# Kernel optimization log

Hardware: AMD Instinct MI355X
Metric: run time of the kernel (lower is better)

Reference implementation:

```python
import jax, jax.numpy as jnp
import numpy as np


def setup_inputs() -> dict:
    key = jax.random.key(0)
    k1, k2, k3 = jax.random.split(key, 3)
    B, F0, D = 8192, 39, 16
    L = 128
    hash_x = jax.random.normal(k1, (B, F0, D), dtype=jnp.float32)
    W0 = jax.random.normal(k2, (F0 * F0, L), dtype=jnp.float32) * 0.05
    W1 = jax.random.normal(k3, (F0 * (L // 2), L), dtype=jnp.float32) * 0.05
    return {"hash_x": hash_x, "W0": W0, "W1": W1}


def reference(hash_x, W0, W1):
    # CIN (Compressed Interaction Network) with layer sizes [128, 128], no bias.
    x0 = hash_x                      # [B, F0, D]
    B, F0, D = x0.shape
    L = W0.shape[1]                  # 128

    # --- layer 0 ---
    # outer product over fields per embedding dim: [B, D, F0, F0] -> flatten (i,j) row-major
    z0 = jnp.einsum('bid,bjd->bdij', x0, x0).reshape(B, D, F0 * F0)
    # conv1d with kernel width 1 == matmul over flattened field-pair dim
    cur0 = jax.nn.relu(jnp.einsum('bdk,kl->bld', z0, W0))   # [B, L, D]
    next_h, direct0 = jnp.split(cur0, 2, axis=1)            # each [B, L/2, D]

    # --- layer 1 (final) ---
    Fk = next_h.shape[1]                                     # L/2 = 64
    z1 = jnp.einsum('bid,bjd->bdij', x0, next_h).reshape(B, D, F0 * Fk)
    cur1 = jax.nn.relu(jnp.einsum('bdk,kl->bld', z1, W1))   # [B, L, D]

    result = jnp.concatenate([direct0, cur1], axis=1)        # [B, L/2 + L, D]
    return jnp.sum(result, axis=-1)                          # [B, 192]
```

## Files before the change

### kernel.cpp

```cpp
#include <hip/hip_runtime.h>
#include <hip/hip_bf16.h>


using short8 = __attribute__((ext_vector_type(8))) short;
using f32x4  = __attribute__((ext_vector_type(4))) float;

#define ZSTR 168
#define V_OFF 0
#define Z_OFF 20480
#define H_OFF (20480 + 43008)
#define SMEM_BYTES (20480 + 43008 + 16384)

#define W0_SLICES 50
#define W1_SLICES 80
#define W0PK_ELEMS (W0_SLICES * 8 * 64 * 8)

__device__ __forceinline__ unsigned short f2bf(float x) {
  __hip_bfloat16 h = __float2bfloat16(x);
  return __builtin_bit_cast(unsigned short, h);
}
__device__ __forceinline__ float bf2f(unsigned short b) {
  unsigned int u = ((unsigned int)b) << 16;
  return __builtin_bit_cast(float, u);
}

__global__ void pack_w(const float* __restrict__ W0, const float* __restrict__ W1,
                       unsigned short* __restrict__ wpk) {
  int tid = blockIdx.x * 256 + threadIdx.x;
  if (tid < W0PK_ELEMS) {
    int p = tid >> 7, n = tid & 127;
    int q = p / 160, rem = p - q * 160;
    int ib = rem / 40, j = rem - ib * 40;
    int i = q * 4 + ib;
    float val = (i < 39 && j < 39) ? W0[(i * 39 + j) * 128 + n] : 0.f;
    int s = p >> 5, kl = p & 31;
    int lane = ((kl >> 3) << 4) | (n & 15);
    int ii = kl & 7, nb = n >> 4;
    wpk[((s * 8 + nb) * 64 + lane) * 8 + ii] = f2bf(val);
  } else {
    int t = tid - W0PK_ELEMS;
    if (t < 2560 * 128) {
      int p = t >> 7, n = t & 127;
      int i = p >> 6, j = p & 63;
      float val = (i < 39) ? W1[(i * 64 + j) * 128 + n] : 0.f;
      int s = p >> 5, kl = p & 31;
      int lane = ((kl >> 3) << 4) | (n & 15);
      int ii = kl & 7, nb = n >> 4;
      wpk[W0PK_ELEMS + ((s * 8 + nb) * 64 + lane) * 8 + ii] = f2bf(val);
    }
  }
}

__global__ __launch_bounds__(256) void cin_main(const float* __restrict__ X,
                                                const short8* __restrict__ wpk,
                                                float* __restrict__ out) {
  extern __shared__ char smem[];
  float* V          = (float*)(smem + V_OFF);
  unsigned short* Z = (unsigned short*)(smem + Z_OFF);
  unsigned short* H = (unsigned short*)(smem + H_OFF);

  const int t    = threadIdx.x;
  const int lane = t & 63;
  const int w    = t >> 6;
  const int wm   = w >> 1, wn = w & 1;
  const int l15  = lane & 15, l4 = lane >> 4;
  const int b0   = blockIdx.x * 8;

  const float* xb = X + (size_t)b0 * 624;
  for (int f = t * 4; f < 4992; f += 1024) {
    float4 v4 = *(const float4*)(xb + f);
    int bl = f / 624;
    int rem = f - bl * 624;
    int i = rem >> 4, d0 = rem & 15;
    int r = bl * 16 + d0;
    V[(r + 0) * 40 + i] = v4.x;
    V[(r + 1) * 40 + i] = v4.y;
    V[(r + 2) * 40 + i] = v4.z;
    V[(r + 3) * 40 + i] = v4.w;
  }
  __syncthreads();

  const int rg = t >> 1, hf = t & 1;

  float vj[20];
  #pragma unroll
  for (int jj = 0; jj < 20; jj++) {
    int j = hf * 20 + jj;
    vj[jj] = (j < 39) ? V[rg * 40 + j] : 0.f;
  }

  f32x4 acc[4][4];
  #pragma unroll
  for (int mi = 0; mi < 4; mi++)
    #pragma unroll
    for (int ni = 0; ni < 4; ni++)
      acc[mi][ni] = (f32x4){0.f, 0.f, 0.f, 0.f};

  for (int q = 0; q < 10; q++) {
    __syncthreads();
    #pragma unroll
    for (int ib = 0; ib < 4; ib++) {
      int i = q * 4 + ib;
      float vi = (i < 39) ? V[rg * 40 + i] : 0.f;
      #pragma unroll
      for (int g = 0; g < 5; g++) {
        ushort4 pk;
        pk.x = f2bf(vi * vj[g * 4 + 0]);
        pk.y = f2bf(vi * vj[g * 4 + 1]);
        pk.z = f2bf(vi * vj[g * 4 + 2]);
        pk.w = f2bf(vi * vj[g * 4 + 3]);
        *(ushort4*)(&Z[rg * ZSTR + ib * 40 + hf * 20 + g * 4]) = pk;
      }
    }
    __syncthreads();
    #pragma unroll
    for (int ss = 0; ss < 5; ss++) {
      int s = q * 5 + ss;
      short8 a[4];
      #pragma unroll
      for (int mi = 0; mi < 4; mi++) {
        int row = wm * 64 + mi * 16 + l15;
        a[mi] = *(const short8*)(&Z[row * ZSTR + ss * 32 + l4 * 8]);
      }
      #pragma unroll
      for (int ni = 0; ni < 4; ni++) {
        short8 bfrag = wpk[(s * 8 + wn * 4 + ni) * 64 + lane];
        #pragma unroll
        for (int mi = 0; mi < 4; mi++)
          acc[mi][ni] = __builtin_amdgcn_mfma_f32_16x16x32_bf16(a[mi], bfrag, acc[mi][ni], 0, 0, 0);
      }
    }
  }

  if (wn == 0) {
    #pragma unroll
    for (int mi = 0; mi < 4; mi++)
      #pragma unroll
      for (int ni = 0; ni < 4; ni++)
        #pragma unroll
        for (int e = 0; e < 4; e++) {
          int row = wm * 64 + mi * 16 + l4 * 4 + e;
          int col = ni * 16 + l15;
          H[row * 64 + col] = f2bf(fmaxf(acc[mi][ni][e], 0.f));
        }
  } else {
    #pragma unroll
    for (int mi = 0; mi < 4; mi++)
      #pragma unroll
      for (int ni = 0; ni < 4; ni++) {
        float s = fmaxf(acc[mi][ni][0], 0.f) + fmaxf(acc[mi][ni][1], 0.f)
                + fmaxf(acc[mi][ni][2], 0.f) + fmaxf(acc[mi][ni][3], 0.f);
        s += __shfl_xor(s, 16);
        s += __shfl_xor(s, 32);
        if (lane < 16)
          out[(size_t)(b0 + wm * 4 + mi) * 192 + ni * 16 + lane] = s;
      }
  }
  __syncthreads();

  #pragma unroll
  for (int mi = 0; mi < 4; mi++)
    #pragma unroll
    for (int ni = 0; ni < 4; ni++)
      acc[mi][ni] = (f32x4){0.f, 0.f, 0.f, 0.f};

  float hj[32];
  #pragma unroll
  for (int g = 0; g < 8; g++) {
    ushort4 pk = *(const ushort4*)(&H[rg * 64 + hf * 32 + g * 4]);
    hj[g * 4 + 0] = bf2f(pk.x);
    hj[g * 4 + 1] = bf2f(pk.y);
    hj[g * 4 + 2] = bf2f(pk.z);
    hj[g * 4 + 3] = bf2f(pk.w);
  }

  for (int q = 0; q < 20; q++) {
    __syncthreads();
    #pragma unroll
    for (int ib = 0; ib < 2; ib++) {
      int i = q * 2 + ib;
      float vi = (i < 39) ? V[rg * 40 + i] : 0.f;
      #pragma unroll
      for (int g = 0; g < 8; g++) {
        ushort4 pk;
        pk.x = f2bf(vi * hj[g * 4 + 0]);
        pk.y = f2bf(vi * hj[g * 4 + 1]);
        pk.z = f2bf(vi * hj[g * 4 + 2]);
        pk.w = f2bf(vi * hj[g * 4 + 3]);
        *(ushort4*)(&Z[rg * ZSTR + ib * 64 + hf * 32 + g * 4]) = pk;
      }
    }
    __syncthreads();
    #pragma unroll
    for (int ss = 0; ss < 4; ss++) {
      int s = W0_SLICES + q * 4 + ss;
      short8 a[4];
      #pragma unroll
      for (int mi = 0; mi < 4; mi++) {
        int row = wm * 64 + mi * 16 + l15;
        a[mi] = *(const short8*)(&Z[row * ZSTR + ss * 32 + l4 * 8]);
      }
      #pragma unroll
      for (int ni = 0; ni < 4; ni++) {
        short8 bfrag = wpk[(s * 8 + wn * 4 + ni) * 64 + lane];
        #pragma unroll
        for (int mi = 0; mi < 4; mi++)
          acc[mi][ni] = __builtin_amdgcn_mfma_f32_16x16x32_bf16(a[mi], bfrag, acc[mi][ni], 0, 0, 0);
      }
    }
  }

  #pragma unroll
  for (int mi = 0; mi < 4; mi++)
    #pragma unroll
    for (int ni = 0; ni < 4; ni++) {
      float s = fmaxf(acc[mi][ni][0], 0.f) + fmaxf(acc[mi][ni][1], 0.f)
              + fmaxf(acc[mi][ni][2], 0.f) + fmaxf(acc[mi][ni][3], 0.f);
      s += __shfl_xor(s, 16);
      s += __shfl_xor(s, 32);
      if (lane < 16)
        out[(size_t)(b0 + wm * 4 + mi) * 192 + 64 + wn * 64 + ni * 16 + lane] = s;
    }
}

extern "C" void kernel_launch(void* const* d_in, const int* in_sizes, int n_in,
                              void* d_out, int out_size, void* d_ws, size_t ws_size,
                              hipStream_t stream) {
  const float* X  = (const float*)d_in[0];
  const float* W0 = (const float*)d_in[1];
  const float* W1 = (const float*)d_in[2];
  float* out = (float*)d_out;
  unsigned short* wpk = (unsigned short*)d_ws;

  (void)hipFuncSetAttribute((const void*)cin_main,
                            hipFuncAttributeMaxDynamicSharedMemorySize, SMEM_BYTES);

  int total_pack = W0PK_ELEMS + W1_SLICES * 8 * 64 * 8;
  pack_w<<<(total_pack + 255) / 256, 256, 0, stream>>>(W0, W1, wpk);
  cin_main<<<1024, 256, SMEM_BYTES, stream>>>(X, (const short8*)wpk, out);
}
```

Measured before the change: 228.4 us.

## Shrink LDS footprint, reblock K loop, swizzle Z tile and pack bf16 conversions

Reorganises the K dimension of both layers: layer 0 now pads j to 48 (60 slices), and layer 1 drops the padded 40th field (78 slices). LDS is reduced by aliasing H onto the Z buffer and using a smaller, XOR-swizzled Z pitch, with launch bounds set to allow 3 blocks per CU. The outer-product generation now uses packed bf16 conversion with 16-byte stores, and the weight pack kernel writes whole fragments at once. The goal is higher occupancy, fewer bank conflicts, less conversion work and fewer wasted MFMAs. In exchange, layer 0 does more padded work, each loop iteration is shorter so there are more barriers, and register pressure rises under the new bound.

```diff
diff --git a/kernel.cpp b/kernel.cpp
--- a/kernel.cpp
+++ b/kernel.cpp
@@ -5,59 +5,61 @@
 using short8 = __attribute__((ext_vector_type(8))) short;
 using f32x4  = __attribute__((ext_vector_type(4))) float;
 
-#define ZSTR 168
-#define V_OFF 0
-#define Z_OFF 20480
-#define H_OFF (20480 + 43008)
-#define SMEM_BYTES (20480 + 43008 + 16384)
-
-#define W0_SLICES 50
-#define W1_SLICES 80
-#define W0PK_ELEMS (W0_SLICES * 8 * 64 * 8)
+#define VSTR    41
+#define V_BYTES (128 * VSTR * 4)
+#define ZPITCH  208
+#define Z_BYTES (128 * ZPITCH)
+#define SMEM_BYTES (V_BYTES + Z_BYTES)
+#define HSTR    68
+
+#define NS0 60
+#define NS1 78
+#define NFRAG ((NS0 + NS1) * 8 * 64)
 
 __device__ __forceinline__ unsigned short f2bf(float x) {
   __hip_bfloat16 h = __float2bfloat16(x);
   return __builtin_bit_cast(unsigned short, h);
 }
-__device__ __forceinline__ float bf2f(unsigned short b) {
-  unsigned int u = ((unsigned int)b) << 16;
-  return __builtin_bit_cast(float, u);
+__device__ __forceinline__ unsigned cvt2(float lo, float hi) {
+  unsigned r;
+  asm("v_cvt_pk_bf16_f32 %0, %1, %2" : "=v"(r) : "v"(lo), "v"(hi));
+  return r;
 }
 
 __global__ void pack_w(const float* __restrict__ W0, const float* __restrict__ W1,
-                       unsigned short* __restrict__ wpk) {
-  int tid = blockIdx.x * 256 + threadIdx.x;
-  if (tid < W0PK_ELEMS) {
-    int p = tid >> 7, n = tid & 127;
-    int q = p / 160, rem = p - q * 160;
-    int ib = rem / 40, j = rem - ib * 40;
-    int i = q * 4 + ib;
-    float val = (i < 39 && j < 39) ? W0[(i * 39 + j) * 128 + n] : 0.f;
-    int s = p >> 5, kl = p & 31;
-    int lane = ((kl >> 3) << 4) | (n & 15);
-    int ii = kl & 7, nb = n >> 4;
-    wpk[((s * 8 + nb) * 64 + lane) * 8 + ii] = f2bf(val);
-  } else {
-    int t = tid - W0PK_ELEMS;
-    if (t < 2560 * 128) {
-      int p = t >> 7, n = t & 127;
-      int i = p >> 6, j = p & 63;
-      float val = (i < 39) ? W1[(i * 64 + j) * 128 + n] : 0.f;
-      int s = p >> 5, kl = p & 31;
-      int lane = ((kl >> 3) << 4) | (n & 15);
-      int ii = kl & 7, nb = n >> 4;
-      wpk[W0PK_ELEMS + ((s * 8 + nb) * 64 + lane) * 8 + ii] = f2bf(val);
-    }
-  }
-}
-
-__global__ __launch_bounds__(256) void cin_main(const float* __restrict__ X,
-                                                const short8* __restrict__ wpk,
-                                                float* __restrict__ out) {
+                       short8* __restrict__ wpk) {
+  int fid = blockIdx.x * 256 + threadIdx.x;
+  if (fid >= NFRAG) return;
+  int lane = fid & 63;
+  int t2 = fid >> 6;
+  int nb = t2 & 7, s = t2 >> 3;
+  int n = nb * 16 + (lane & 15);
+  int klb = (lane >> 4) * 8;
+  short8 frag;
+  #pragma unroll
+  for (int ii = 0; ii < 8; ii++) {
+    float val;
+    if (s < NS0) {
+      int k = s * 32 + klb + ii;
+      int i = k / 48, j = k - i * 48;
+      val = (i < 39 && j < 39) ? W0[(i * 39 + j) * 128 + n] : 0.f;
+    } else {
+      int k = (s - NS0) * 32 + klb + ii;
+      int i = k >> 6, j = k & 63;
+      val = W1[(i * 64 + j) * 128 + n];
+    }
+    frag[ii] = (short)f2bf(val);
+  }
+  wpk[fid] = frag;
+}
+
+__global__ __launch_bounds__(256, 3) void cin_main(const float* __restrict__ X,
+                                                   const short8* __restrict__ wpk,
+                                                   float* __restrict__ out) {
   extern __shared__ char smem[];
-  float* V          = (float*)(smem + V_OFF);
-  unsigned short* Z = (unsigned short*)(smem + Z_OFF);
-  unsigned short* H = (unsigned short*)(smem + H_OFF);
+  float* V          = (float*)smem;
+  char*  Zc         = smem + V_BYTES;
+  unsigned short* H = (unsigned short*)(smem + V_BYTES);
 
   const int t    = threadIdx.x;
   const int lane = t & 63;
@@ -73,20 +75,30 @@
     int rem = f - bl * 624;
     int i = rem >> 4, d0 = rem & 15;
     int r = bl * 16 + d0;
-    V[(r + 0) * 40 + i] = v4.x;
-    V[(r + 1) * 40 + i] = v4.y;
-    V[(r + 2) * 40 + i] = v4.z;
-    V[(r + 3) * 40 + i] = v4.w;
-  }
+    V[(r + 0) * VSTR + i] = v4.x;
+    V[(r + 1) * VSTR + i] = v4.y;
+    V[(r + 2) * VSTR + i] = v4.z;
+    V[(r + 3) * VSTR + i] = v4.w;
+  }
+  if (t < 128) V[t * VSTR + 39] = 0.f;
   __syncthreads();
 
   const int rg = t >> 1, hf = t & 1;
-
-  float vj[20];
-  #pragma unroll
-  for (int jj = 0; jj < 20; jj++) {
-    int j = hf * 20 + jj;
-    vj[jj] = (j < 39) ? V[rg * 40 + j] : 0.f;
+  const unsigned zrow = (unsigned)rg * ZPITCH;
+  const unsigned zxor = (unsigned)((rg >> 3) & 1) << 4;
+
+  unsigned abase[4];
+  #pragma unroll
+  for (int mi = 0; mi < 4; mi++) {
+    int row = wm * 64 + mi * 16 + l15;
+    abase[mi] = ((unsigned)row * ZPITCH + (unsigned)l4 * 16) ^ ((unsigned)((row >> 3) & 1) << 4);
+  }
+
+  float vj[24];
+  #pragma unroll
+  for (int jj = 0; jj < 24; jj++) {
+    int j = hf * 24 + jj;
+    vj[jj] = (j < 39) ? V[rg * VSTR + j] : 0.f;
   }
 
   f32x4 acc[4][4];
@@ -96,32 +108,30 @@
     for (int ni = 0; ni < 4; ni++)
       acc[mi][ni] = (f32x4){0.f, 0.f, 0.f, 0.f};
 
-  for (int q = 0; q < 10; q++) {
-    __syncthreads();
-    #pragma unroll
-    for (int ib = 0; ib < 4; ib++) {
-      int i = q * 4 + ib;
-      float vi = (i < 39) ? V[rg * 40 + i] : 0.f;
-      #pragma unroll
-      for (int g = 0; g < 5; g++) {
-        ushort4 pk;
-        pk.x = f2bf(vi * vj[g * 4 + 0]);
-        pk.y = f2bf(vi * vj[g * 4 + 1]);
-        pk.z = f2bf(vi * vj[g * 4 + 2]);
-        pk.w = f2bf(vi * vj[g * 4 + 3]);
-        *(ushort4*)(&Z[rg * ZSTR + ib * 40 + hf * 20 + g * 4]) = pk;
-      }
-    }
-    __syncthreads();
-    #pragma unroll
-    for (int ss = 0; ss < 5; ss++) {
-      int s = q * 5 + ss;
+  #pragma unroll 1
+  for (int q = 0; q < 20; q++) {
+    #pragma unroll
+    for (int ib = 0; ib < 2; ib++) {
+      float vi = V[rg * VSTR + (2 * q + ib)];
+      #pragma unroll
+      for (int g = 0; g < 3; g++) {
+        float p0 = vi * vj[g * 8 + 0], p1 = vi * vj[g * 8 + 1];
+        float p2 = vi * vj[g * 8 + 2], p3 = vi * vj[g * 8 + 3];
+        float p4 = vi * vj[g * 8 + 4], p5 = vi * vj[g * 8 + 5];
+        float p6 = vi * vj[g * 8 + 6], p7 = vi * vj[g * 8 + 7];
+        uint4 pk = { cvt2(p0, p1), cvt2(p2, p3), cvt2(p4, p5), cvt2(p6, p7) };
+        unsigned off = (zrow + (unsigned)(ib * 96 + hf * 48 + g * 16)) ^ zxor;
+        *(uint4*)(Zc + off) = pk;
+      }
+    }
+    __syncthreads();
+    #pragma unroll
+    for (int ss = 0; ss < 3; ss++) {
+      int s = q * 3 + ss;
       short8 a[4];
       #pragma unroll
-      for (int mi = 0; mi < 4; mi++) {
-        int row = wm * 64 + mi * 16 + l15;
-        a[mi] = *(const short8*)(&Z[row * ZSTR + ss * 32 + l4 * 8]);
-      }
+      for (int mi = 0; mi < 4; mi++)
+        a[mi] = *(const short8*)(Zc + abase[mi] + (unsigned)ss * 64);
       #pragma unroll
       for (int ni = 0; ni < 4; ni++) {
         short8 bfrag = wpk[(s * 8 + wn * 4 + ni) * 64 + lane];
@@ -130,6 +140,7 @@
           acc[mi][ni] = __builtin_amdgcn_mfma_f32_16x16x32_bf16(a[mi], bfrag, acc[mi][ni], 0, 0, 0);
       }
     }
+    __syncthreads();
   }
 
   if (wn == 0) {
@@ -141,7 +152,7 @@
         for (int e = 0; e < 4; e++) {
           int row = wm * 64 + mi * 16 + l4 * 4 + e;
           int col = ni * 16 + l15;
-          H[row * 64 + col] = f2bf(fmaxf(acc[mi][ni][e], 0.f));
+          H[row * HSTR + col] = f2bf(fmaxf(acc[mi][ni][e], 0.f));
         }
   } else {
     #pragma unroll
@@ -158,48 +169,46 @@
   }
   __syncthreads();
 
+  float hj[32];
+  #pragma unroll
+  for (int g = 0; g < 8; g++) {
+    ushort4 pk = *(const ushort4*)(&H[rg * HSTR + hf * 32 + g * 4]);
+    hj[g * 4 + 0] = ((float)0.f, __builtin_bit_cast(float, (unsigned)pk.x << 16));
+    hj[g * 4 + 1] = __builtin_bit_cast(float, (unsigned)pk.y << 16);
+    hj[g * 4 + 2] = __builtin_bit_cast(float, (unsigned)pk.z << 16);
+    hj[g * 4 + 3] = __builtin_bit_cast(float, (unsigned)pk.w << 16);
+  }
+  __syncthreads();
+
   #pragma unroll
   for (int mi = 0; mi < 4; mi++)
     #pragma unroll
     for (int ni = 0; ni < 4; ni++)
       acc[mi][ni] = (f32x4){0.f, 0.f, 0.f, 0.f};
 
-  float hj[32];
-  #pragma unroll
-  for (int g = 0; g < 8; g++) {
-    ushort4 pk = *(const ushort4*)(&H[rg * 64 + hf * 32 + g * 4]);
-    hj[g * 4 + 0] = bf2f(pk.x);
-    hj[g * 4 + 1] = bf2f(pk.y);
-    hj[g * 4 + 2] = bf2f(pk.z);
-    hj[g * 4 + 3] = bf2f(pk.w);
-  }
-
-  for (int q = 0; q < 20; q++) {
-    __syncthreads();
-    #pragma unroll
-    for (int ib = 0; ib < 2; ib++) {
-      int i = q * 2 + ib;
-      float vi = (i < 39) ? V[rg * 40 + i] : 0.f;
-      #pragma unroll
-      for (int g = 0; g < 8; g++) {
-        ushort4 pk;
-        pk.x = f2bf(vi * hj[g * 4 + 0]);
-        pk.y = f2bf(vi * hj[g * 4 + 1]);
-        pk.z = f2bf(vi * hj[g * 4 + 2]);
-        pk.w = f2bf(vi * hj[g * 4 + 3]);
-        *(ushort4*)(&Z[rg * ZSTR + ib * 64 + hf * 32 + g * 4]) = pk;
-      }
-    }
-    __syncthreads();
-    #pragma unroll
-    for (int ss = 0; ss < 4; ss++) {
-      int s = W0_SLICES + q * 4 + ss;
+  #pragma unroll 1
+  for (int q = 0; q < 39; q++) {
+    {
+      float vi = V[rg * VSTR + q];
+      #pragma unroll
+      for (int g = 0; g < 4; g++) {
+        float p0 = vi * hj[g * 8 + 0], p1 = vi * hj[g * 8 + 1];
+        float p2 = vi * hj[g * 8 + 2], p3 = vi * hj[g * 8 + 3];
+        float p4 = vi * hj[g * 8 + 4], p5 = vi * hj[g * 8 + 5];
+        float p6 = vi * hj[g * 8 + 6], p7 = vi * hj[g * 8 + 7];
+        uint4 pk = { cvt2(p0, p1), cvt2(p2, p3), cvt2(p4, p5), cvt2(p6, p7) };
+        unsigned off = (zrow + (unsigned)(hf * 64 + g * 16)) ^ zxor;
+        *(uint4*)(Zc + off) = pk;
+      }
+    }
+    __syncthreads();
+    #pragma unroll
+    for (int ss = 0; ss < 2; ss++) {
+      int s = NS0 + q * 2 + ss;
       short8 a[4];
       #pragma unroll
-      for (int mi = 0; mi < 4; mi++) {
-        int row = wm * 64 + mi * 16 + l15;
-        a[mi] = *(const short8*)(&Z[row * ZSTR + ss * 32 + l4 * 8]);
-      }
+      for (int mi = 0; mi < 4; mi++)
+        a[mi] = *(const short8*)(Zc + abase[mi] + (unsigned)ss * 64);
       #pragma unroll
       for (int ni = 0; ni < 4; ni++) {
         short8 bfrag = wpk[(s * 8 + wn * 4 + ni) * 64 + lane];
@@ -208,6 +217,7 @@
           acc[mi][ni] = __builtin_amdgcn_mfma_f32_16x16x32_bf16(a[mi], bfrag, acc[mi][ni], 0, 0, 0);
       }
     }
+    __syncthreads();
   }
 
   #pragma unroll
@@ -226,16 +236,13 @@
 extern "C" void kernel_launch(void* const* d_in, const int* in_sizes, int n_in,
                               void* d_out, int out_size, void* d_ws, size_t ws_size,
                               hipStream_t stream) {
+  (void)in_sizes; (void)n_in; (void)out_size; (void)ws_size;
   const float* X  = (const float*)d_in[0];
   const float* W0 = (const float*)d_in[1];
   const float* W1 = (const float*)d_in[2];
   float* out = (float*)d_out;
-  unsigned short* wpk = (unsigned short*)d_ws;
-
-  (void)hipFuncSetAttribute((const void*)cin_main,
-                            hipFuncAttributeMaxDynamicSharedMemorySize, SMEM_BYTES);
-
-  int total_pack = W0PK_ELEMS + W1_SLICES * 8 * 64 * 8;
-  pack_w<<<(total_pack + 255) / 256, 256, 0, stream>>>(W0, W1, wpk);
-  cin_main<<<1024, 256, SMEM_BYTES, stream>>>(X, (const short8*)wpk, out);
-}
+  short8* wpk = (short8*)d_ws;
+
+  pack_w<<<(NFRAG + 255) / 256, 256, 0, stream>>>(W0, W1, wpk);
+  cin_main<<<1024, 256, SMEM_BYTES, stream>>>(X, wpk, out);
+}
```

Measured after the change: 240.9 us. 1.05x slower.
